# Optimization experiments

Measured on AMD Instinct MI355X. Metric: run time of the kernel, lower is better.

The kernel has to match this reference:

```python
import jax, jax.numpy as jnp
import numpy as np

EPS = 1e-12  # F.normalize default eps

def _l2_normalize(x, axis):
    # matches torch F.normalize: x / max(||x||_2, eps)
    n = jnp.sqrt(jnp.sum(x * x, axis=axis, keepdims=True))
    return x / jnp.maximum(n, EPS)

def setup_inputs() -> dict:
    key = jax.random.key(0)
    k1, k2 = jax.random.split(key)
    N, B, C = 4096, 16, 512
    x_pre = jax.random.normal(k1, (N, B, C), dtype=jnp.float32)
    x_pos = jax.random.normal(k2, (N, B, C), dtype=jnp.float32)
    return {"x_pre": x_pre, "x_pos": x_pos}

def reference(x_pre, x_pos):
    # [N, B, C]
    fea_pred = _l2_normalize(x_pre, axis=2)
    fea_later = _l2_normalize(x_pos, axis=2)
    # Original does a full bmm [B, N, N] then takes the diagonal; the diagonal
    # is just the per-token dot product (cosine similarity). Same math.
    dis = jnp.sum(fea_pred * fea_later, axis=2, keepdims=True)  # [N, B, 1]
    weight = 1.0 - jax.nn.sigmoid(dis)
    return x_pos * weight
```

## Files before the change

kernel.cpp:

```cpp
#include <hip/hip_runtime.h>


constexpr int C_DIM = 512;
constexpr int ROWS  = 4096 * 16;

__device__ __forceinline__ void partials(const float4& p, const float4& q,
                                         float& s_pre, float& s_pos, float& dot) {
    s_pre = fmaf(p.x, p.x, s_pre); s_pre = fmaf(p.y, p.y, s_pre);
    s_pre = fmaf(p.z, p.z, s_pre); s_pre = fmaf(p.w, p.w, s_pre);
    s_pos = fmaf(q.x, q.x, s_pos); s_pos = fmaf(q.y, q.y, s_pos);
    s_pos = fmaf(q.z, q.z, s_pos); s_pos = fmaf(q.w, q.w, s_pos);
    dot   = fmaf(p.x, q.x, dot);   dot   = fmaf(p.y, q.y, dot);
    dot   = fmaf(p.z, q.z, dot);   dot   = fmaf(p.w, q.w, dot);
}

__global__ __launch_bounds__(256) void tokenmixer_kernel(
    const float* __restrict__ pre,
    const float* __restrict__ pos,
    float* __restrict__ out)
{
    const int wave = (int)((blockIdx.x * 256u + threadIdx.x) >> 6);
    const int lane = (int)(threadIdx.x & 63u);

    const size_t b = (size_t)wave * (2 * C_DIM) + (size_t)lane * 4;

    const float4 p0 = *reinterpret_cast<const float4*>(pre + b);
    const float4 p1 = *reinterpret_cast<const float4*>(pre + b + 256);
    const float4 p2 = *reinterpret_cast<const float4*>(pre + b + 512);
    const float4 p3 = *reinterpret_cast<const float4*>(pre + b + 768);
    const float4 q0 = *reinterpret_cast<const float4*>(pos + b);
    const float4 q1 = *reinterpret_cast<const float4*>(pos + b + 256);
    const float4 q2 = *reinterpret_cast<const float4*>(pos + b + 512);
    const float4 q3 = *reinterpret_cast<const float4*>(pos + b + 768);

    float sp0 = 0.f, sq0 = 0.f, d0 = 0.f;
    float sp1 = 0.f, sq1 = 0.f, d1 = 0.f;
    partials(p0, q0, sp0, sq0, d0);
    partials(p1, q1, sp0, sq0, d0);
    partials(p2, q2, sp1, sq1, d1);
    partials(p3, q3, sp1, sq1, d1);

#pragma unroll
    for (int m = 1; m < 64; m <<= 1) {
        sp0 += __shfl_xor(sp0, m, 64);
        sq0 += __shfl_xor(sq0, m, 64);
        d0  += __shfl_xor(d0,  m, 64);
        sp1 += __shfl_xor(sp1, m, 64);
        sq1 += __shfl_xor(sq1, m, 64);
        d1  += __shfl_xor(d1,  m, 64);
    }

    const float c0 = d0 / (fmaxf(sqrtf(sp0), 1e-12f) * fmaxf(sqrtf(sq0), 1e-12f));
    const float c1 = d1 / (fmaxf(sqrtf(sp1), 1e-12f) * fmaxf(sqrtf(sq1), 1e-12f));
    const float w0 = 1.0f / (1.0f + __expf(c0));
    const float w1 = 1.0f / (1.0f + __expf(c1));

    float4 o;
    o.x = q0.x * w0; o.y = q0.y * w0; o.z = q0.z * w0; o.w = q0.w * w0;
    *reinterpret_cast<float4*>(out + b) = o;
    o.x = q1.x * w0; o.y = q1.y * w0; o.z = q1.z * w0; o.w = q1.w * w0;
    *reinterpret_cast<float4*>(out + b + 256) = o;
    o.x = q2.x * w1; o.y = q2.y * w1; o.z = q2.z * w1; o.w = q2.w * w1;
    *reinterpret_cast<float4*>(out + b + 512) = o;
    o.x = q3.x * w1; o.y = q3.y * w1; o.z = q3.z * w1; o.w = q3.w * w1;
    *reinterpret_cast<float4*>(out + b + 768) = o;
}

extern "C" void kernel_launch(void* const* d_in, const int* in_sizes, int n_in,
                              void* d_out, int out_size, void* d_ws, size_t ws_size,
                              hipStream_t stream) {
    const float* pre = (const float*)d_in[0];
    const float* pos = (const float*)d_in[1];
    float* out = (float*)d_out;

    const int blocks = ROWS / 8;
    tokenmixer_kernel<<<blocks, 256, 0, stream>>>(pre, pos, out);
}
```

Before: 306.0 us.

## Process four row pairs per wave with double-buffered prefetch and nontemporal stores

Each wave now handles four consecutive row-pairs instead of one, prefetching the next pair's inputs into registers while it reduces and writes the current one. Output stores use nontemporal hints to avoid polluting caches. The grid shrinks fourfold. This aims to hide memory latency and reduce launch and block overhead, at the cost of more registers per thread and fewer resident waves.

```diff
diff --git a/kernel.cpp b/kernel.cpp
--- a/kernel.cpp
+++ b/kernel.cpp
@@ -3,6 +3,22 @@
 
 constexpr int C_DIM = 512;
 constexpr int ROWS  = 4096 * 16;
+constexpr int ITERS = 4;
+
+typedef float f32x4 __attribute__((ext_vector_type(4)));
+
+__device__ __forceinline__ void load4(const float* __restrict__ p, size_t b,
+                                      float4 v[4]) {
+    v[0] = *reinterpret_cast<const float4*>(p + b);
+    v[1] = *reinterpret_cast<const float4*>(p + b + 256);
+    v[2] = *reinterpret_cast<const float4*>(p + b + 512);
+    v[3] = *reinterpret_cast<const float4*>(p + b + 768);
+}
+
+__device__ __forceinline__ void store_nt(float* p, float4 v) {
+    __builtin_nontemporal_store(*reinterpret_cast<f32x4*>(&v),
+                                reinterpret_cast<f32x4*>(p));
+}
 
 __device__ __forceinline__ void partials(const float4& p, const float4& q,
                                          float& s_pre, float& s_pos, float& dot) {
@@ -22,48 +38,59 @@
     const int wave = (int)((blockIdx.x * 256u + threadIdx.x) >> 6);
     const int lane = (int)(threadIdx.x & 63u);
 
-    const size_t b = (size_t)wave * (2 * C_DIM) + (size_t)lane * 4;
+    const size_t base = (size_t)wave * (ITERS * 2 * C_DIM) + (size_t)lane * 4;
 
-    const float4 p0 = *reinterpret_cast<const float4*>(pre + b);
-    const float4 p1 = *reinterpret_cast<const float4*>(pre + b + 256);
-    const float4 p2 = *reinterpret_cast<const float4*>(pre + b + 512);
-    const float4 p3 = *reinterpret_cast<const float4*>(pre + b + 768);
-    const float4 q0 = *reinterpret_cast<const float4*>(pos + b);
-    const float4 q1 = *reinterpret_cast<const float4*>(pos + b + 256);
-    const float4 q2 = *reinterpret_cast<const float4*>(pos + b + 512);
-    const float4 q3 = *reinterpret_cast<const float4*>(pos + b + 768);
-
-    float sp0 = 0.f, sq0 = 0.f, d0 = 0.f;
-    float sp1 = 0.f, sq1 = 0.f, d1 = 0.f;
-    partials(p0, q0, sp0, sq0, d0);
-    partials(p1, q1, sp0, sq0, d0);
-    partials(p2, q2, sp1, sq1, d1);
-    partials(p3, q3, sp1, sq1, d1);
+    float4 P[2][4], Q[2][4];
+    load4(pre, base, P[0]);
+    load4(pos, base, Q[0]);
 
 #pragma unroll
-    for (int m = 1; m < 64; m <<= 1) {
-        sp0 += __shfl_xor(sp0, m, 64);
-        sq0 += __shfl_xor(sq0, m, 64);
-        d0  += __shfl_xor(d0,  m, 64);
-        sp1 += __shfl_xor(sp1, m, 64);
-        sq1 += __shfl_xor(sq1, m, 64);
-        d1  += __shfl_xor(d1,  m, 64);
+    for (int k = 0; k < ITERS; ++k) {
+        const int cur = k & 1;
+        const int nxt = cur ^ 1;
+        const size_t cb = base + (size_t)k * (2 * C_DIM);
+
+        if (k + 1 < ITERS) {
+            load4(pre, cb + 2 * C_DIM, P[nxt]);
+            load4(pos, cb + 2 * C_DIM, Q[nxt]);
+        }
+
+        float sp0 = 0.f, sq0 = 0.f, d0 = 0.f;
+        float sp1 = 0.f, sq1 = 0.f, d1 = 0.f;
+        partials(P[cur][0], Q[cur][0], sp0, sq0, d0);
+        partials(P[cur][1], Q[cur][1], sp0, sq0, d0);
+        partials(P[cur][2], Q[cur][2], sp1, sq1, d1);
+        partials(P[cur][3], Q[cur][3], sp1, sq1, d1);
+
+#pragma unroll
+        for (int m = 1; m < 64; m <<= 1) {
+            sp0 += __shfl_xor(sp0, m, 64);
+            sq0 += __shfl_xor(sq0, m, 64);
+            d0  += __shfl_xor(d0,  m, 64);
+            sp1 += __shfl_xor(sp1, m, 64);
+            sq1 += __shfl_xor(sq1, m, 64);
+            d1  += __shfl_xor(d1,  m, 64);
+        }
+
+        const float c0 = d0 / (fmaxf(sqrtf(sp0), 1e-12f) * fmaxf(sqrtf(sq0), 1e-12f));
+        const float c1 = d1 / (fmaxf(sqrtf(sp1), 1e-12f) * fmaxf(sqrtf(sq1), 1e-12f));
+        const float w0 = 1.0f / (1.0f + __expf(c0));
+        const float w1 = 1.0f / (1.0f + __expf(c1));
+
+        float4 o;
+        o.x = Q[cur][0].x * w0; o.y = Q[cur][0].y * w0;
+        o.z = Q[cur][0].z * w0; o.w = Q[cur][0].w * w0;
+        store_nt(out + cb, o);
+        o.x = Q[cur][1].x * w0; o.y = Q[cur][1].y * w0;
+        o.z = Q[cur][1].z * w0; o.w = Q[cur][1].w * w0;
+        store_nt(out + cb + 256, o);
+        o.x = Q[cur][2].x * w1; o.y = Q[cur][2].y * w1;
+        o.z = Q[cur][2].z * w1; o.w = Q[cur][2].w * w1;
+        store_nt(out + cb + 512, o);
+        o.x = Q[cur][3].x * w1; o.y = Q[cur][3].y * w1;
+        o.z = Q[cur][3].z * w1; o.w = Q[cur][3].w * w1;
+        store_nt(out + cb + 768, o);
     }
-
-    const float c0 = d0 / (fmaxf(sqrtf(sp0), 1e-12f) * fmaxf(sqrtf(sq0), 1e-12f));
-    const float c1 = d1 / (fmaxf(sqrtf(sp1), 1e-12f) * fmaxf(sqrtf(sq1), 1e-12f));
-    const float w0 = 1.0f / (1.0f + __expf(c0));
-    const float w1 = 1.0f / (1.0f + __expf(c1));
-
-    float4 o;
-    o.x = q0.x * w0; o.y = q0.y * w0; o.z = q0.z * w0; o.w = q0.w * w0;
-    *reinterpret_cast<float4*>(out + b) = o;
-    o.x = q1.x * w0; o.y = q1.y * w0; o.z = q1.z * w0; o.w = q1.w * w0;
-    *reinterpret_cast<float4*>(out + b + 256) = o;
-    o.x = q2.x * w1; o.y = q2.y * w1; o.z = q2.z * w1; o.w = q2.w * w1;
-    *reinterpret_cast<float4*>(out + b + 512) = o;
-    o.x = q3.x * w1; o.y = q3.y * w1; o.z = q3.z * w1; o.w = q3.w * w1;
-    *reinterpret_cast<float4*>(out + b + 768) = o;
 }
 
 extern "C" void kernel_launch(void* const* d_in, const int* in_sizes, int n_in,
@@ -73,6 +100,6 @@
     const float* pos = (const float*)d_in[1];
     float* out = (float*)d_out;
 
-    const int blocks = ROWS / 8;
+    const int blocks = ROWS / 32;
     tokenmixer_kernel<<<blocks, 256, 0, stream>>>(pre, pos, out);
 }
```

Result: slower. 320.2 us (+4.6%).
